# Optimization experiments

Measured on AMD Instinct MI355X. Metric: run time of the kernel, lower is better.

Reference implementation:

```python
import jax, jax.numpy as jnp
import numpy as np

T, B, OBS, HID = 64, 1024, 8, 512
N_ODE_STEPS = 4  # fixed-step RK4 over t in [0, 1]
LN_EPS = 1e-5


def _ln(x, g, b):
    m = x.mean(-1, keepdims=True)
    v = ((x - m) ** 2).mean(-1, keepdims=True)
    return (x - m) / jnp.sqrt(v + LN_EPS) * g + b


def setup_inputs() -> dict:
    key = jax.random.key(0)
    ks = jax.random.split(key, 24)

    def w(k, shape, fan_in):
        s = 1.0 / np.sqrt(fan_in)
        return jax.random.uniform(k, shape, jnp.float32, -s, s)

    return {
        "xs": jax.random.normal(ks[0], (T, B, OBS), jnp.float32),
        # obs2hidden MLP: Linear + LayerNorm + LeakyReLU
        "obs_W": w(ks[1], (OBS, HID), OBS),
        "obs_b": w(ks[2], (HID,), OBS),
        "obs_ln_g": jnp.ones((HID,), jnp.float32),
        "obs_ln_b": jnp.zeros((HID,), jnp.float32),
        # ODE func MLP (time-concat input, 2 hidden layers, linear out)
        "ode_W1": w(ks[3], (HID + 1, HID), HID + 1),
        "ode_b1": w(ks[4], (HID,), HID + 1),
        "ode_ln1_g": jnp.ones((HID,), jnp.float32),
        "ode_ln1_b": jnp.zeros((HID,), jnp.float32),
        "ode_W2": w(ks[5], (HID, HID), HID),
        "ode_b2": w(ks[6], (HID,), HID),
        "ode_ln2_g": jnp.ones((HID,), jnp.float32),
        "ode_ln2_b": jnp.zeros((HID,), jnp.float32),
        "ode_Wout": w(ks[7], (HID, HID), HID),
        "ode_bout": w(ks[8], (HID,), HID),
        # GRU cell (torch gate order: r, z, n)
        "W_ih": w(ks[9], (HID, 3 * HID), HID),
        "b_ih": w(ks[10], (3 * HID,), HID),
        "W_hh": w(ks[11], (HID, 3 * HID), HID),
        "b_hh": w(ks[12], (3 * HID,), HID),
    }


def reference(xs, obs_W, obs_b, obs_ln_g, obs_ln_b,
              ode_W1, ode_b1, ode_ln1_g, ode_ln1_b,
              ode_W2, ode_b2, ode_ln2_g, ode_ln2_b,
              ode_Wout, ode_bout, W_ih, b_ih, W_hh, b_hh):
    batch = xs.shape[1]

    # obs -> hidden for all timesteps at once: [T, B, HID]
    hs = jax.nn.leaky_relu(_ln(xs @ obs_W + obs_b, obs_ln_g, obs_ln_b))

    def ode_f(h, t):  # h: [B, HID], t: scalar
        ht = jnp.concatenate([h, jnp.full((batch, 1), t, h.dtype)], axis=-1)
        z = jax.nn.leaky_relu(_ln(ht @ ode_W1 + ode_b1, ode_ln1_g, ode_ln1_b))
        z = jax.nn.leaky_relu(_ln(z @ ode_W2 + ode_b2, ode_ln2_g, ode_ln2_b))
        return z @ ode_Wout + ode_bout

    dt = 1.0 / N_ODE_STEPS

    def rk4_solve(h0):
        def body(h, t):
            k1 = ode_f(h, t)
            k2 = ode_f(h + 0.5 * dt * k1, t + 0.5 * dt)
            k3 = ode_f(h + 0.5 * dt * k2, t + 0.5 * dt)
            k4 = ode_f(h + dt * k3, t + dt)
            return h + (dt / 6.0) * (k1 + 2 * k2 + 2 * k3 + k4), None
        ts = jnp.arange(N_ODE_STEPS, dtype=h0.dtype) * dt
        h, _ = jax.lax.scan(body, h0, ts)
        return h

    def gru_cell(x, h):
        gi = x @ W_ih + b_ih
        gh = h @ W_hh + b_hh
        i_r, i_z, i_n = jnp.split(gi, 3, axis=-1)
        h_r, h_z, h_n = jnp.split(gh, 3, axis=-1)
        r = jax.nn.sigmoid(i_r + h_r)
        z = jax.nn.sigmoid(i_z + h_z)
        n = jnp.tanh(i_n + r * h_n)
        return (1.0 - z) * n + z * h

    def step(h_prev, h_obs):
        h_ode = rk4_solve(h_obs)          # NeuralODE: integrate from t=0 to 1
        h_new = gru_cell(h_ode, h_prev)   # GRU step
        return h_new, None

    h0 = jnp.zeros((batch, hs.shape[-1]), hs.dtype)
    h_final, _ = jax.lax.scan(step, h0, hs)
    return h_final  # [B, HID]
```

## Files before the change

kernel.cpp:

```cpp
#include <hip/hip_runtime.h>
#include <stdint.h>


typedef __bf16 bf16x8 __attribute__((ext_vector_type(8)));
typedef float floatx4 __attribute__((ext_vector_type(4)));

#define AP 520
#define KSR 257
#define REDW 9

static __device__ __forceinline__ float bf2f(unsigned short u) {
  union { unsigned int u32; float f; } c;
  c.u32 = ((unsigned int)u) << 16;
  return c.f;
}
static __device__ __forceinline__ unsigned short f2bf(float f) {
  union { __bf16 h; unsigned short u; } c;
  c.h = (__bf16)f;
  return c.u;
}
static __device__ __forceinline__ unsigned int pk2(float a, float b) {
  return (unsigned int)f2bf(a) | ((unsigned int)f2bf(b) << 16);
}

static __device__ __forceinline__ void barrier_lds() {
  __asm__ volatile("s_waitcnt lgkmcnt(0)\n\ts_barrier" ::: "memory");
}

__global__ void tile_weight(const float* __restrict__ src, unsigned short* __restrict__ dst) {
  int t = blockIdx.x * 256 + threadIdx.x;
  int ml = t & 15, qd = (t >> 4) & 3;
  int nt = (t >> 6) & 31, kk = t >> 11;
  int n = nt * 16 + ml;
  int k0 = kk * 32 + qd * 8;
  unsigned short o[8] __attribute__((aligned(16)));
#pragma unroll
  for (int j = 0; j < 8; ++j) o[j] = f2bf(src[(size_t)(k0 + j) * 512 + n]);
  *(uint4*)(dst + (size_t)t * 8) = *(const uint4*)o;
}

__global__ void transpose_f2b(const float* __restrict__ src, unsigned short* __restrict__ dst,
                              int R, int C) {
  __shared__ float t[32][33];
  int c0 = blockIdx.x * 32, r0 = blockIdx.y * 32;
  int tx = threadIdx.x, ty = threadIdx.y;
#pragma unroll
  for (int i = 0; i < 32; i += 8) t[ty + i][tx] = src[(size_t)(r0 + ty + i) * C + c0 + tx];
  __syncthreads();
#pragma unroll
  for (int i = 0; i < 32; i += 8) dst[(size_t)(c0 + ty + i) * R + r0 + tx] = f2bf(t[tx][ty + i]);
}

__global__ __launch_bounds__(256) void obs_embed(
    const float* __restrict__ xs, const float* __restrict__ W,
    const float* __restrict__ bias, const float* __restrict__ gam,
    const float* __restrict__ bet, unsigned short* __restrict__ Y) {
  __shared__ float Wl[4096];
  const int tid = threadIdx.x, lane = tid & 63, wv = tid >> 6;
#pragma unroll
  for (int i = 0; i < 16; ++i) Wl[i * 256 + tid] = W[i * 256 + tid];
  __syncthreads();
  size_t row = (size_t)blockIdx.x * 4 + wv;
  float xf[8];
  {
    const float* xp = xs + row * 8;
#pragma unroll
    for (int k = 0; k < 8; ++k) xf[k] = xp[k];
  }
  int n0 = lane * 8;
  float a[8];
#pragma unroll
  for (int j = 0; j < 8; ++j) a[j] = bias[n0 + j];
#pragma unroll
  for (int k = 0; k < 8; ++k)
#pragma unroll
    for (int j = 0; j < 8; ++j) a[j] += xf[k] * Wl[k * 512 + n0 + j];
  float s1 = 0.f, s2 = 0.f;
#pragma unroll
  for (int j = 0; j < 8; ++j) { s1 += a[j]; s2 += a[j] * a[j]; }
#pragma unroll
  for (int off = 1; off < 64; off <<= 1) { s1 += __shfl_xor(s1, off); s2 += __shfl_xor(s2, off); }
  float mean = s1 * (1.f / 512.f);
  float rstd = rsqrtf(s2 * (1.f / 512.f) - mean * mean + 1e-5f);
  unsigned short o[8] __attribute__((aligned(16)));
#pragma unroll
  for (int j = 0; j < 8; ++j) {
    float v = (a[j] - mean) * rstd * gam[n0 + j] + bet[n0 + j];
    v = v > 0.f ? v : 0.01f * v;
    o[j] = f2bf(v);
  }
  *(uint4*)(Y + row * 512 + n0) = *(const uint4*)o;
}


static __device__ __forceinline__ int a_addr(int row, int n) {
  return (((row >> 4) * 16 + (n >> 5)) * 4 + ((n >> 3) & 3)) * 128 + (row & 15) * 8 + (n & 7);
}

static __device__ __forceinline__ void bload(const unsigned short* __restrict__ Wt, int kk,
                                             int wvoff, bf16x8 (&b)[4]) {
  const unsigned short* p = Wt + (size_t)kk * 16384 + wvoff;
#pragma unroll
  for (int j = 0; j < 4; ++j) b[j] = *(const bf16x8*)(p + j * 512);
}

static __device__ __forceinline__ void gemmS(const unsigned short* __restrict__ Wt,
                                             const unsigned short* __restrict__ Wnext,
                                             const unsigned short* As, int wvoff, int lane,
                                             const floatx4 (&bias)[4],
                                             bf16x8 (&bb)[2][4], floatx4 (&acc)[4][4]) {
#pragma unroll
  for (int mi = 0; mi < 4; ++mi)
#pragma unroll
    for (int j = 0; j < 4; ++j) acc[mi][j] = bias[j];
#pragma unroll 2
  for (int kk = 0; kk < 16; ++kk) {
#pragma unroll
    for (int mh = 0; mh < 2; ++mh) {
      bf16x8 a0 = *(const bf16x8*)&As[((2 * mh) * 16 + kk) * 512 + lane * 8];
      bf16x8 a1 = *(const bf16x8*)&As[((2 * mh + 1) * 16 + kk) * 512 + lane * 8];
#pragma unroll
      for (int j = 0; j < 4; ++j) {
        acc[2 * mh][j] =
            __builtin_amdgcn_mfma_f32_16x16x32_bf16(bb[kk & 1][j], a0, acc[2 * mh][j], 0, 0, 0);
        acc[2 * mh + 1][j] =
            __builtin_amdgcn_mfma_f32_16x16x32_bf16(bb[kk & 1][j], a1, acc[2 * mh + 1][j], 0, 0, 0);
      }
    }
    if (kk < 14) bload(Wt, kk + 2, wvoff, bb[kk & 1]);
    else bload(Wnext, kk - 14, wvoff, bb[kk & 1]);
  }
}

static __device__ __forceinline__ void ln_epi(floatx4 (&acc)[4][4], unsigned short* As,
                                              const float* Pg, const float* Pb,
                                              int wv, int lane, float2* red) {
  const int ml = lane & 15, qd = lane >> 4;
#pragma unroll
  for (int mi = 0; mi < 4; ++mi) {
    float s1 = 0.f, s2 = 0.f;
#pragma unroll
    for (int j = 0; j < 4; ++j)
#pragma unroll
      for (int r = 0; r < 4; ++r) { float x = acc[mi][j][r]; s1 += x; s2 += x * x; }
    s1 += __shfl_xor(s1, 16); s2 += __shfl_xor(s2, 16);
    s1 += __shfl_xor(s1, 32); s2 += __shfl_xor(s2, 32);
    if (qd == 0) red[(mi * 16 + ml) * REDW + wv] = make_float2(s1, s2);
  }
  barrier_lds();
  float mean[4], rstd[4];
#pragma unroll
  for (int mi = 0; mi < 4; ++mi) {
    float S1 = 0.f, S2 = 0.f;
#pragma unroll
    for (int w = 0; w < 8; ++w) {
      float2 v = red[(mi * 16 + ml) * REDW + w];
      S1 += v.x; S2 += v.y;
    }
    float m = S1 * (1.f / 512.f);
    mean[mi] = m;
    rstd[mi] = rsqrtf(S2 * (1.f / 512.f) - m * m + 1e-5f);
  }
#pragma unroll
  for (int j = 0; j < 4; ++j) {
    int nb = (4 * wv + j) * 16 + qd * 4;
    floatx4 gm = *(const floatx4*)&Pg[nb];
    floatx4 bt = *(const floatx4*)&Pb[nb];
#pragma unroll
    for (int mi = 0; mi < 4; ++mi) {
      float x0 = (acc[mi][j][0] - mean[mi]) * rstd[mi] * gm[0] + bt[0];
      float x1 = (acc[mi][j][1] - mean[mi]) * rstd[mi] * gm[1] + bt[1];
      float x2 = (acc[mi][j][2] - mean[mi]) * rstd[mi] * gm[2] + bt[2];
      float x3 = (acc[mi][j][3] - mean[mi]) * rstd[mi] * gm[3] + bt[3];
      x0 = x0 > 0.f ? x0 : 0.01f * x0;
      x1 = x1 > 0.f ? x1 : 0.01f * x1;
      x2 = x2 > 0.f ? x2 : 0.01f * x2;
      x3 = x3 > 0.f ? x3 : 0.01f * x3;
      uint2 o = make_uint2(pk2(x0, x1), pk2(x2, x3));
      *(uint2*)(As + a_addr(mi * 16 + ml, nb)) = o;
    }
  }
  barrier_lds();
}

static __device__ __forceinline__ void stage_epi(floatx4 (&acc)[4][4], float (&h)[4][4][4],
                                                 unsigned int* Ks, unsigned short* As,
                                                 unsigned short* Yb, size_t m0,
                                                 int stg, bool last, int wv, int lane) {
  const int ml = lane & 15, qd = lane >> 4;
  barrier_lds();
#pragma unroll
  for (int mi = 0; mi < 4; ++mi) {
    int rowK = (mi * 16 + ml) * KSR;
#pragma unroll
    for (int j = 0; j < 4; ++j) {
      int nb = (4 * wv + j) * 16 + qd * 4;
      unsigned int yw[2];
#pragma unroll
      for (int p = 0; p < 2; ++p) {
        int kidx = rowK + (4 * wv + j) * 8 + qd * 2 + p;
        float kv0 = acc[mi][j][2 * p];
        float kv1 = acc[mi][j][2 * p + 1];
        unsigned int pk = (stg != 0) ? Ks[kidx] : 0u;
        float s0 = bf2f((unsigned short)(pk & 0xffffu));
        float s1 = bf2f((unsigned short)(pk >> 16));
        float h0 = h[mi][j][2 * p], h1 = h[mi][j][2 * p + 1];
        float y0, y1;
        if (stg == 0)      { s0 = kv0;        s1 = kv1;        y0 = h0 + 0.125f * kv0; y1 = h1 + 0.125f * kv1; }
        else if (stg == 1) { s0 += 2.f * kv0; s1 += 2.f * kv1; y0 = h0 + 0.125f * kv0; y1 = h1 + 0.125f * kv1; }
        else if (stg == 2) { s0 += 2.f * kv0; s1 += 2.f * kv1; y0 = h0 + 0.25f * kv0;  y1 = h1 + 0.25f * kv1; }
        else {
          h0 += (1.f / 24.f) * (s0 + kv0);
          h1 += (1.f / 24.f) * (s1 + kv1);
          h[mi][j][2 * p] = h0; h[mi][j][2 * p + 1] = h1;
          y0 = h0; y1 = h1;
        }
        if (stg != 3) Ks[kidx] = pk2(s0, s1);
        yw[p] = pk2(y0, y1);
      }
      uint2 o = make_uint2(yw[0], yw[1]);
      *(uint2*)(As + a_addr(mi * 16 + ml, nb)) = o;
      if (last && stg == 3)
        *(uint2*)(Yb + (m0 + mi * 16 + ml) * 512 + nb) = o;
    }
  }
  barrier_lds();
}

__global__ __launch_bounds__(512) void ode_mega(
    unsigned short* Yb, const unsigned short* __restrict__ W1t,
    const unsigned short* __restrict__ W2t, const unsigned short* __restrict__ Wot,
    const float* __restrict__ b1, const float* __restrict__ tr, const float* __restrict__ g1,
    const float* __restrict__ be1, const float* __restrict__ b2, const float* __restrict__ g2,
    const float* __restrict__ be2, const float* __restrict__ bo) {
  __shared__ __align__(16) unsigned short As[32768];
  __shared__ __align__(16) float Pf[8 * 512];
  __shared__ float2 red[64 * REDW];
  __shared__ __align__(16) unsigned int Ks[64 * KSR];

  const int tid = threadIdx.x;
  const int lane = tid & 63;
  const int wv = tid >> 6;
  const int ml = lane & 15;
  const int qd = lane >> 4;
  const size_t m0 = (size_t)blockIdx.x * 64;
  const int wvoff = wv * 2048 + lane * 8;

  bf16x8 bb[2][4];
  bload(W1t, 0, wvoff, bb[0]);
  bload(W1t, 1, wvoff, bb[1]);

  {
    const float* srcs[8] = {b1, tr, g1, be1, b2, g2, be2, bo};
#pragma unroll
    for (int v = 0; v < 8; ++v) Pf[v * 512 + tid] = srcs[v][tid];
  }

  {
    int r = tid >> 3;
    int c0 = tid & 7;
#pragma unroll
    for (int i = 0; i < 8; ++i) {
      int c = c0 + i * 8;
      uint4 v = *(const uint4*)(Yb + (m0 + r) * 512 + c * 8);
      int dst = (((r >> 4) * 16 + (c >> 2)) * 4 + (c & 3)) * 128 + (r & 15) * 8;
      *(uint4*)(As + dst) = v;
    }
  }
  barrier_lds();

  float h[4][4][4];
#pragma unroll
  for (int mi = 0; mi < 4; ++mi)
#pragma unroll
    for (int j = 0; j < 4; ++j) {
      int nb = (4 * wv + j) * 16 + qd * 4;
      uint2 v = *(const uint2*)(As + a_addr(mi * 16 + ml, nb));
      h[mi][j][0] = bf2f((unsigned short)(v.x & 0xffffu));
      h[mi][j][1] = bf2f((unsigned short)(v.x >> 16));
      h[mi][j][2] = bf2f((unsigned short)(v.y & 0xffffu));
      h[mi][j][3] = bf2f((unsigned short)(v.y >> 16));
    }

  for (int e = 0; e < 16; ++e) {
    int stg = e & 3;
    float tval = 0.25f * (float)(e >> 2) + ((stg == 3) ? 0.25f : (stg ? 0.125f : 0.f));
    floatx4 acc[4][4];
    floatx4 bias[4];

#pragma unroll
    for (int j = 0; j < 4; ++j) {
      int nb = (4 * wv + j) * 16 + qd * 4;
      floatx4 vb = *(const floatx4*)&Pf[0 * 512 + nb];
      floatx4 vt = *(const floatx4*)&Pf[1 * 512 + nb];
#pragma unroll
      for (int r = 0; r < 4; ++r) bias[j][r] = vb[r] + tval * vt[r];
    }
    gemmS(W1t, W2t, As, wvoff, lane, bias, bb, acc);
    ln_epi(acc, As, Pf + 2 * 512, Pf + 3 * 512, wv, lane, red);

#pragma unroll
    for (int j = 0; j < 4; ++j) {
      int nb = (4 * wv + j) * 16 + qd * 4;
      bias[j] = *(const floatx4*)&Pf[4 * 512 + nb];
    }
    gemmS(W2t, Wot, As, wvoff, lane, bias, bb, acc);
    ln_epi(acc, As, Pf + 5 * 512, Pf + 6 * 512, wv, lane, red);

#pragma unroll
    for (int j = 0; j < 4; ++j) {
      int nb = (4 * wv + j) * 16 + qd * 4;
      bias[j] = *(const floatx4*)&Pf[7 * 512 + nb];
    }
    gemmS(Wot, W1t, As, wvoff, lane, bias, bb, acc);
    stage_epi(acc, h, Ks, As, Yb, m0, stg, e == 15, wv, lane);
  }
}

__global__ __launch_bounds__(256) void gru_step(
    const unsigned short* __restrict__ Yt, const float* __restrict__ hprev,
    float* __restrict__ hnew, const unsigned short* __restrict__ Wiht,
    const unsigned short* __restrict__ Whht, const float* __restrict__ bih,
    const float* __restrict__ bhh) {
  __shared__ __align__(16) unsigned short Ay[32 * AP];
  __shared__ __align__(16) unsigned short Ah[32 * AP];
  const int tid = threadIdx.x, lane = tid & 63, wv = tid >> 6;
  const int ml = lane & 15, qd = lane >> 4;
  const int m0 = blockIdx.x * 32;
  const int j0 = blockIdx.y * 64;

  const unsigned short* bp[6];
#pragma unroll
  for (int g = 0; g < 6; ++g) {
    const unsigned short* mat = (g < 3) ? Wiht : Whht;
    int gate = (g < 3) ? g : (g - 3);
    bp[g] = mat + (size_t)(gate * 512 + j0 + 16 * wv + ml) * 512 + qd * 8;
  }
  bf16x8 bgl[2][6];
#pragma unroll
  for (int g = 0; g < 6; ++g) bgl[0][g] = *(const bf16x8*)(bp[g]);
#pragma unroll
  for (int g = 0; g < 6; ++g) bgl[1][g] = *(const bf16x8*)(bp[g] + 32);

  {
    int r = tid >> 3, c0 = tid & 7;
#pragma unroll
    for (int i = 0; i < 8; ++i) {
      int c = c0 + i * 8;
      *(uint4*)(Ay + r * AP + c * 8) = *(const uint4*)(Yt + (size_t)(m0 + r) * 512 + c * 8);
    }
#pragma unroll
    for (int i = 0; i < 8; ++i) {
      int c = c0 + i * 8;
      const float* s = hprev + (size_t)(m0 + r) * 512 + c * 8;
      unsigned short o[8] __attribute__((aligned(16)));
#pragma unroll
      for (int j = 0; j < 8; ++j) o[j] = f2bf(s[j]);
      *(uint4*)(Ah + r * AP + c * 8) = *(const uint4*)o;
    }
  }
  __syncthreads();

  floatx4 acc[2][6];
#pragma unroll
  for (int mi = 0; mi < 2; ++mi)
#pragma unroll
    for (int g = 0; g < 6; ++g) acc[mi][g] = 0.f;

#pragma unroll 2
  for (int kk = 0; kk < 16; ++kk) {
    bf16x8 ay[2], ah[2];
#pragma unroll
    for (int mi = 0; mi < 2; ++mi) {
      ay[mi] = *(const bf16x8*)&Ay[(16 * mi + ml) * AP + kk * 32 + qd * 8];
      ah[mi] = *(const bf16x8*)&Ah[(16 * mi + ml) * AP + kk * 32 + qd * 8];
    }
#pragma unroll
    for (int g = 0; g < 6; ++g) {
#pragma unroll
      for (int mi = 0; mi < 2; ++mi)
        acc[mi][g] = __builtin_amdgcn_mfma_f32_16x16x32_bf16((g < 3) ? ay[mi] : ah[mi],
                                                             bgl[kk & 1][g], acc[mi][g], 0, 0, 0);
    }
    if (kk < 14) {
#pragma unroll
      for (int g = 0; g < 6; ++g) bgl[kk & 1][g] = *(const bf16x8*)(bp[g] + (kk + 2) * 32);
    }
  }

  int j = j0 + 16 * wv + ml;
  float bi_r = bih[j], bi_z = bih[512 + j], bi_n = bih[1024 + j];
  float bh_r = bhh[j], bh_z = bhh[512 + j], bh_n = bhh[1024 + j];
#pragma unroll
  for (int mi = 0; mi < 2; ++mi)
#pragma unroll
    for (int r = 0; r < 4; ++r) {
      size_t row = (size_t)(m0 + 16 * mi + 4 * qd + r);
      float rg = acc[mi][0][r] + bi_r + acc[mi][3][r] + bh_r;
      rg = 1.f / (1.f + __expf(-rg));
      float zg = acc[mi][1][r] + bi_z + acc[mi][4][r] + bh_z;
      zg = 1.f / (1.f + __expf(-zg));
      float ng = tanhf(acc[mi][2][r] + bi_n + rg * (acc[mi][5][r] + bh_n));
      float hp = hprev[row * 512 + j];
      hnew[row * 512 + j] = (1.f - zg) * ng + zg * hp;
    }
}

__global__ void zero_h(float* hf) {
  int i = blockIdx.x * 256 + threadIdx.x;
  hf[i] = 0.f;
}

extern "C" void kernel_launch(void* const* d_in, const int* in_sizes, int n_in,
                              void* d_out, int out_size, void* d_ws, size_t ws_size,
                              hipStream_t stream) {
  (void)in_sizes; (void)n_in; (void)out_size; (void)ws_size;
  const float* xs    = (const float*)d_in[0];
  const float* obsW  = (const float*)d_in[1];
  const float* obsb  = (const float*)d_in[2];
  const float* obsg  = (const float*)d_in[3];
  const float* obsbe = (const float*)d_in[4];
  const float* W1    = (const float*)d_in[5];
  const float* b1    = (const float*)d_in[6];
  const float* g1    = (const float*)d_in[7];
  const float* be1   = (const float*)d_in[8];
  const float* W2    = (const float*)d_in[9];
  const float* b2    = (const float*)d_in[10];
  const float* g2    = (const float*)d_in[11];
  const float* be2   = (const float*)d_in[12];
  const float* Wo    = (const float*)d_in[13];
  const float* bo    = (const float*)d_in[14];
  const float* Wih   = (const float*)d_in[15];
  const float* bih   = (const float*)d_in[16];
  const float* Whh   = (const float*)d_in[17];
  const float* bhh   = (const float*)d_in[18];

  char* p = (char*)d_ws;
  auto take = [&](size_t bytes) { char* q = p; p += (bytes + 255) & ~(size_t)255; return q; };
  unsigned short* W1t  = (unsigned short*)take((size_t)512 * 512 * 2);
  unsigned short* W2t  = (unsigned short*)take((size_t)512 * 512 * 2);
  unsigned short* Wot  = (unsigned short*)take((size_t)512 * 512 * 2);
  unsigned short* Wiht = (unsigned short*)take((size_t)1536 * 512 * 2);
  unsigned short* Whht = (unsigned short*)take((size_t)1536 * 512 * 2);
  float* hf0 = (float*)take((size_t)1024 * 512 * 4);
  float* hf1 = (float*)take((size_t)1024 * 512 * 4);
  unsigned short* Yb = (unsigned short*)take((size_t)65536 * 512 * 2);

  dim3 tb(32, 8);
  tile_weight<<<128, 256, 0, stream>>>(W1, W1t);
  tile_weight<<<128, 256, 0, stream>>>(W2, W2t);
  tile_weight<<<128, 256, 0, stream>>>(Wo, Wot);
  transpose_f2b<<<dim3(48, 16), tb, 0, stream>>>(Wih, Wiht, 512, 1536);
  transpose_f2b<<<dim3(48, 16), tb, 0, stream>>>(Whh, Whht, 512, 1536);

  obs_embed<<<16384, 256, 0, stream>>>(xs, obsW, obsb, obsg, obsbe, Yb);

  ode_mega<<<1024, 512, 0, stream>>>(Yb, W1t, W2t, Wot, b1, W1 + 512 * 512, g1, be1, b2, g2,
                                     be2, bo);

  zero_h<<<2048, 256, 0, stream>>>(hf0);
  float* hf[2] = {hf0, hf1};
  for (int t = 0; t < 64; ++t) {
    int s = t & 1, d = s ^ 1;
    float* hn = (t == 63) ? (float*)d_out : hf[d];
    gru_step<<<dim3(32, 8), 256, 0, stream>>>(Yb + (size_t)t * 1024 * 512, hf[s], hn, Wiht, Whht,
                                              bih, bhh);
  }
}
```

Before: 2.885 ms.

## Fuse GRU time loop into one cooperative kernel with grid sync

Replaces the 64 separate gru_step launches and the zero_h kernel with a single cooperative kernel that loops over timesteps and uses grid.sync between steps, treating t=0 as zero hidden state. It also widens LDS accesses in the ODE epilogues: the reduction reads become float4 and the RK4 accumulator reads and writes become uint2, with padding changes to keep them aligned. The aim is to remove per-step launch overhead and cut LDS instruction count, at the cost of grid-wide barrier latency and a dependence on all 256 blocks being co-resident.

```diff
diff --git a/kernel.cpp b/kernel.cpp
--- a/kernel.cpp
+++ b/kernel.cpp
@@ -1,4 +1,5 @@
 #include <hip/hip_runtime.h>
+#include <hip/hip_cooperative_groups.h>
 #include <stdint.h>
 
 
@@ -6,8 +7,8 @@
 typedef float floatx4 __attribute__((ext_vector_type(4)));
 
 #define AP 520
-#define KSR 257
-#define REDW 9
+#define KSR 258
+#define REDW 10
 
 static __device__ __forceinline__ float bf2f(unsigned short u) {
   union { unsigned int u32; float f; } c;
@@ -151,12 +152,10 @@
   float mean[4], rstd[4];
 #pragma unroll
   for (int mi = 0; mi < 4; ++mi) {
-    float S1 = 0.f, S2 = 0.f;
-#pragma unroll
-    for (int w = 0; w < 8; ++w) {
-      float2 v = red[(mi * 16 + ml) * REDW + w];
-      S1 += v.x; S2 += v.y;
-    }
+    const float4* rp = (const float4*)&red[(mi * 16 + ml) * REDW];
+    float4 a0 = rp[0], a1 = rp[1], a2 = rp[2], a3 = rp[3];
+    float S1 = a0.x + a0.z + a1.x + a1.z + a2.x + a2.z + a3.x + a3.z;
+    float S2 = a0.y + a0.w + a1.y + a1.w + a2.y + a2.w + a3.y + a3.w;
     float m = S1 * (1.f / 512.f);
     mean[mi] = m;
     rstd[mi] = rsqrtf(S2 * (1.f / 512.f) - m * m + 1e-5f);
@@ -195,13 +194,14 @@
 #pragma unroll
     for (int j = 0; j < 4; ++j) {
       int nb = (4 * wv + j) * 16 + qd * 4;
-      unsigned int yw[2];
+      int kbase = rowK + (4 * wv + j) * 8 + qd * 2;
+      uint2 pks = (stg != 0) ? *(const uint2*)&Ks[kbase] : make_uint2(0u, 0u);
+      unsigned int yw[2], sw[2];
 #pragma unroll
       for (int p = 0; p < 2; ++p) {
-        int kidx = rowK + (4 * wv + j) * 8 + qd * 2 + p;
+        unsigned int pk = p ? pks.y : pks.x;
         float kv0 = acc[mi][j][2 * p];
         float kv1 = acc[mi][j][2 * p + 1];
-        unsigned int pk = (stg != 0) ? Ks[kidx] : 0u;
         float s0 = bf2f((unsigned short)(pk & 0xffffu));
         float s1 = bf2f((unsigned short)(pk >> 16));
         float h0 = h[mi][j][2 * p], h1 = h[mi][j][2 * p + 1];
@@ -215,9 +215,10 @@
           h[mi][j][2 * p] = h0; h[mi][j][2 * p + 1] = h1;
           y0 = h0; y1 = h1;
         }
-        if (stg != 3) Ks[kidx] = pk2(s0, s1);
+        sw[p] = pk2(s0, s1);
         yw[p] = pk2(y0, y1);
       }
+      if (stg != 3) *(uint2*)&Ks[kbase] = make_uint2(sw[0], sw[1]);
       uint2 o = make_uint2(yw[0], yw[1]);
       *(uint2*)(As + a_addr(mi * 16 + ml, nb)) = o;
       if (last && stg == 3)
@@ -235,7 +236,7 @@
     const float* __restrict__ be2, const float* __restrict__ bo) {
   __shared__ __align__(16) unsigned short As[32768];
   __shared__ __align__(16) float Pf[8 * 512];
-  __shared__ float2 red[64 * REDW];
+  __shared__ __align__(16) float2 red[64 * REDW];
   __shared__ __align__(16) unsigned int Ks[64 * KSR];
 
   const int tid = threadIdx.x;
@@ -317,17 +318,19 @@
   }
 }
 
-__global__ __launch_bounds__(256) void gru_step(
-    const unsigned short* __restrict__ Yt, const float* __restrict__ hprev,
-    float* __restrict__ hnew, const unsigned short* __restrict__ Wiht,
-    const unsigned short* __restrict__ Whht, const float* __restrict__ bih,
-    const float* __restrict__ bhh) {
+__global__ __launch_bounds__(256) void gru_all(
+    const unsigned short* __restrict__ Yb, float* __restrict__ hf0,
+    float* __restrict__ hf1, float* __restrict__ out,
+    const unsigned short* __restrict__ Wiht, const unsigned short* __restrict__ Whht,
+    const float* __restrict__ bih, const float* __restrict__ bhh) {
+  namespace cg = cooperative_groups;
+  cg::grid_group grid = cg::this_grid();
   __shared__ __align__(16) unsigned short Ay[32 * AP];
   __shared__ __align__(16) unsigned short Ah[32 * AP];
   const int tid = threadIdx.x, lane = tid & 63, wv = tid >> 6;
   const int ml = lane & 15, qd = lane >> 4;
-  const int m0 = blockIdx.x * 32;
-  const int j0 = blockIdx.y * 64;
+  const int m0 = (blockIdx.x >> 3) * 32;
+  const int j0 = (blockIdx.x & 7) * 64;
 
   const unsigned short* bp[6];
 #pragma unroll
@@ -336,79 +339,89 @@
     int gate = (g < 3) ? g : (g - 3);
     bp[g] = mat + (size_t)(gate * 512 + j0 + 16 * wv + ml) * 512 + qd * 8;
   }
-  bf16x8 bgl[2][6];
-#pragma unroll
-  for (int g = 0; g < 6; ++g) bgl[0][g] = *(const bf16x8*)(bp[g]);
-#pragma unroll
-  for (int g = 0; g < 6; ++g) bgl[1][g] = *(const bf16x8*)(bp[g] + 32);
-
-  {
-    int r = tid >> 3, c0 = tid & 7;
-#pragma unroll
-    for (int i = 0; i < 8; ++i) {
-      int c = c0 + i * 8;
-      *(uint4*)(Ay + r * AP + c * 8) = *(const uint4*)(Yt + (size_t)(m0 + r) * 512 + c * 8);
-    }
-#pragma unroll
-    for (int i = 0; i < 8; ++i) {
-      int c = c0 + i * 8;
-      const float* s = hprev + (size_t)(m0 + r) * 512 + c * 8;
-      unsigned short o[8] __attribute__((aligned(16)));
-#pragma unroll
-      for (int j = 0; j < 8; ++j) o[j] = f2bf(s[j]);
-      *(uint4*)(Ah + r * AP + c * 8) = *(const uint4*)o;
-    }
-  }
-  __syncthreads();
-
-  floatx4 acc[2][6];
-#pragma unroll
-  for (int mi = 0; mi < 2; ++mi)
-#pragma unroll
-    for (int g = 0; g < 6; ++g) acc[mi][g] = 0.f;
+  const int j = j0 + 16 * wv + ml;
+  const float bi_r = bih[j], bi_z = bih[512 + j], bi_n = bih[1024 + j];
+  const float bh_r = bhh[j], bh_z = bhh[512 + j], bh_n = bhh[1024 + j];
+
+  for (int t = 0; t < 64; ++t) {
+    const unsigned short* Yt = Yb + (size_t)t * 1024 * 512;
+    const float* hprev = (t & 1) ? hf1 : hf0;
+    float* hnew = (t == 63) ? out : ((t & 1) ? hf0 : hf1);
+
+    bf16x8 bgl[2][6];
+#pragma unroll
+    for (int g = 0; g < 6; ++g) bgl[0][g] = *(const bf16x8*)(bp[g]);
+#pragma unroll
+    for (int g = 0; g < 6; ++g) bgl[1][g] = *(const bf16x8*)(bp[g] + 32);
+
+    {
+      int r = tid >> 3, c0 = tid & 7;
+#pragma unroll
+      for (int i = 0; i < 8; ++i) {
+        int c = c0 + i * 8;
+        *(uint4*)(Ay + r * AP + c * 8) = *(const uint4*)(Yt + (size_t)(m0 + r) * 512 + c * 8);
+      }
+      if (t == 0) {
+        uint4 z = make_uint4(0u, 0u, 0u, 0u);
+#pragma unroll
+        for (int i = 0; i < 8; ++i) *(uint4*)(Ah + r * AP + (c0 + i * 8) * 8) = z;
+      } else {
+#pragma unroll
+        for (int i = 0; i < 8; ++i) {
+          int c = c0 + i * 8;
+          const float* s = hprev + (size_t)(m0 + r) * 512 + c * 8;
+          unsigned short o[8] __attribute__((aligned(16)));
+#pragma unroll
+          for (int jj = 0; jj < 8; ++jj) o[jj] = f2bf(s[jj]);
+          *(uint4*)(Ah + r * AP + c * 8) = *(const uint4*)o;
+        }
+      }
+    }
+    __syncthreads();
+
+    floatx4 acc[2][6];
+#pragma unroll
+    for (int mi = 0; mi < 2; ++mi)
+#pragma unroll
+      for (int g = 0; g < 6; ++g) acc[mi][g] = 0.f;
 
 #pragma unroll 2
-  for (int kk = 0; kk < 16; ++kk) {
-    bf16x8 ay[2], ah[2];
-#pragma unroll
-    for (int mi = 0; mi < 2; ++mi) {
-      ay[mi] = *(const bf16x8*)&Ay[(16 * mi + ml) * AP + kk * 32 + qd * 8];
-      ah[mi] = *(const bf16x8*)&Ah[(16 * mi + ml) * AP + kk * 32 + qd * 8];
-    }
-#pragma unroll
-    for (int g = 0; g < 6; ++g) {
-#pragma unroll
-      for (int mi = 0; mi < 2; ++mi)
-        acc[mi][g] = __builtin_amdgcn_mfma_f32_16x16x32_bf16((g < 3) ? ay[mi] : ah[mi],
-                                                             bgl[kk & 1][g], acc[mi][g], 0, 0, 0);
-    }
-    if (kk < 14) {
-#pragma unroll
-      for (int g = 0; g < 6; ++g) bgl[kk & 1][g] = *(const bf16x8*)(bp[g] + (kk + 2) * 32);
-    }
-  }
-
-  int j = j0 + 16 * wv + ml;
-  float bi_r = bih[j], bi_z = bih[512 + j], bi_n = bih[1024 + j];
-  float bh_r = bhh[j], bh_z = bhh[512 + j], bh_n = bhh[1024 + j];
-#pragma unroll
-  for (int mi = 0; mi < 2; ++mi)
-#pragma unroll
-    for (int r = 0; r < 4; ++r) {
-      size_t row = (size_t)(m0 + 16 * mi + 4 * qd + r);
-      float rg = acc[mi][0][r] + bi_r + acc[mi][3][r] + bh_r;
-      rg = 1.f / (1.f + __expf(-rg));
-      float zg = acc[mi][1][r] + bi_z + acc[mi][4][r] + bh_z;
-      zg = 1.f / (1.f + __expf(-zg));
-      float ng = tanhf(acc[mi][2][r] + bi_n + rg * (acc[mi][5][r] + bh_n));
-      float hp = hprev[row * 512 + j];
-      hnew[row * 512 + j] = (1.f - zg) * ng + zg * hp;
-    }
-}
-
-__global__ void zero_h(float* hf) {
-  int i = blockIdx.x * 256 + threadIdx.x;
-  hf[i] = 0.f;
+    for (int kk = 0; kk < 16; ++kk) {
+      bf16x8 ay[2], ah[2];
+#pragma unroll
+      for (int mi = 0; mi < 2; ++mi) {
+        ay[mi] = *(const bf16x8*)&Ay[(16 * mi + ml) * AP + kk * 32 + qd * 8];
+        ah[mi] = *(const bf16x8*)&Ah[(16 * mi + ml) * AP + kk * 32 + qd * 8];
+      }
+#pragma unroll
+      for (int g = 0; g < 6; ++g) {
+#pragma unroll
+        for (int mi = 0; mi < 2; ++mi)
+          acc[mi][g] = __builtin_amdgcn_mfma_f32_16x16x32_bf16(
+              (g < 3) ? ay[mi] : ah[mi], bgl[kk & 1][g], acc[mi][g], 0, 0, 0);
+      }
+      if (kk < 14) {
+#pragma unroll
+        for (int g = 0; g < 6; ++g) bgl[kk & 1][g] = *(const bf16x8*)(bp[g] + (kk + 2) * 32);
+      }
+    }
+
+#pragma unroll
+    for (int mi = 0; mi < 2; ++mi)
+#pragma unroll
+      for (int r = 0; r < 4; ++r) {
+        size_t row = (size_t)(m0 + 16 * mi + 4 * qd + r);
+        float rg = acc[mi][0][r] + bi_r + acc[mi][3][r] + bh_r;
+        rg = 1.f / (1.f + __expf(-rg));
+        float zg = acc[mi][1][r] + bi_z + acc[mi][4][r] + bh_z;
+        zg = 1.f / (1.f + __expf(-zg));
+        float ng = tanhf(acc[mi][2][r] + bi_n + rg * (acc[mi][5][r] + bh_n));
+        float hp = (t == 0) ? 0.f : hprev[row * 512 + j];
+        hnew[row * 512 + j] = (1.f - zg) * ng + zg * hp;
+      }
+
+    grid.sync();
+  }
 }
 
 extern "C" void kernel_launch(void* const* d_in, const int* in_sizes, int n_in,
@@ -458,12 +471,8 @@
   ode_mega<<<1024, 512, 0, stream>>>(Yb, W1t, W2t, Wot, b1, W1 + 512 * 512, g1, be1, b2, g2,
                                      be2, bo);
 
-  zero_h<<<2048, 256, 0, stream>>>(hf0);
-  float* hf[2] = {hf0, hf1};
-  for (int t = 0; t < 64; ++t) {
-    int s = t & 1, d = s ^ 1;
-    float* hn = (t == 63) ? (float*)d_out : hf[d];
-    gru_step<<<dim3(32, 8), 256, 0, stream>>>(Yb + (size_t)t * 1024 * 512, hf[s], hn, Wiht, Whht,
-                                              bih, bhh);
-  }
-}
+  {
+    void* args[] = {&Yb, &hf0, &hf1, &d_out, &Wiht, &Whht, &bih, &bhh};
+    hipLaunchCooperativeKernel((const void*)gru_all, dim3(256), dim3(256), args, 0, stream);
+  }
+}
```

Measured after the change: 4.871 ms. +68.8%, slower.
